# Optimization experiments

Hardware: AMD Instinct MI355X
Metric: run time of the kernel (lower is better)

The kernel has to match this reference:

```python
import jax, jax.numpy as jnp
import numpy as np

B, T, E, H, QKV = 4, 2048, 1024, 16, 64
D = E // H  # head_dim = 64


def setup_inputs() -> dict:
    key = jax.random.key(0)
    k1, k2, k3, k4 = jax.random.split(key, 4)
    scale = 1.0 / np.sqrt(D)
    x = jax.random.normal(k1, (B, T, E), dtype=jnp.float32)
    W_q = jax.random.normal(k2, (QKV, D), dtype=jnp.float32) * scale
    W_k = jax.random.normal(k3, (QKV, D), dtype=jnp.float32) * scale
    W_v = jax.random.normal(k4, (QKV, D), dtype=jnp.float32) * scale
    return {"x": x, "W_q": W_q, "W_k": W_k, "W_v": W_v}


def reference(x, W_q, W_k, W_v):
    Bx, Tx, Ex = x.shape
    d = Ex // H
    # [B,T,E] -> [B,H,T,D]  (same as torch view + permute(0,2,1,3))
    xh = x.reshape(Bx, Tx, H, d).transpose(0, 2, 1, 3)
    # Shared per-head projections: Linear(d -> qkv_dim), weight stored [out,in]
    Q = jnp.einsum("bhtd,qd->bhtq", xh, W_q)
    K = jnp.einsum("bhtd,qd->bhtq", xh, W_k)
    V = jnp.einsum("bhtd,qd->bhtq", xh, W_v)
    # NOTE: original scales by head_dim**0.5, not qkv_dim**0.5
    scores = jnp.einsum("bhtq,bhsq->bhts", Q, K) / jnp.asarray(d, x.dtype) ** 0.5
    attn = jax.nn.softmax(scores, axis=-1)
    out = jnp.einsum("bhts,bhsq->bhtq", attn, V) + V  # attention + V residual
    # per-head concat on last dim == head-major merge: [B,H,T,Q] -> [B,T,H*Q]
    return out.transpose(0, 2, 1, 3).reshape(Bx, Tx, H * W_q.shape[0])
```

## Files before the change

kernel.cpp:

```cpp
#include <hip/hip_runtime.h>

#define T_SEQ 2048
#define N_B   4
#define N_H   16
#define D_H   64
#define EMB   1024
#define CSC   0.18033688011f

typedef __attribute__((ext_vector_type(8))) short   vshort8;
typedef __attribute__((ext_vector_type(4))) float   vfloat4;
typedef __attribute__((ext_vector_type(16))) float  vfloat16;

__device__ __forceinline__ ushort f2bf(float f) {
  union { float f; unsigned u; } v; v.f = f;
  unsigned u = v.u;
  return (ushort)((u + 0x7fffu + ((u >> 16) & 1u)) >> 16);
}
__device__ __forceinline__ unsigned pk2bf(float a, float b) {
  return (unsigned)f2bf(a) | ((unsigned)f2bf(b) << 16);
}
__device__ __forceinline__ float bf2f(ushort b) {
  union { unsigned u; float f; } v; v.u = ((unsigned)b) << 16;
  return v.f;
}
__device__ __forceinline__ float fexp2(float x) {
#if __has_builtin(__builtin_amdgcn_exp2f)
  return __builtin_amdgcn_exp2f(x);
#else
  return exp2f(x);
#endif
}
__device__ __forceinline__ unsigned permhi(float hi, float lo) {
  union { float f; unsigned u; } a, b; a.f = hi; b.f = lo;
#if __has_builtin(__builtin_amdgcn_perm)
  return __builtin_amdgcn_perm(a.u, b.u, 0x07060302u);
#else
  return (a.u & 0xFFFF0000u) | (b.u >> 16);
#endif
}
__device__ __forceinline__ void plswap(unsigned &a, unsigned &b) {
  asm("v_permlane32_swap_b32 %0, %1" : "+v"(a), "+v"(b));
}
__device__ __forceinline__ vshort8 cvt8(const float* p) {
  float4 w0 = *(const float4*)(p);
  float4 w1 = *(const float4*)(p + 4);
  vshort8 t;
  t[0] = (short)f2bf(w0.x); t[1] = (short)f2bf(w0.y);
  t[2] = (short)f2bf(w0.z); t[3] = (short)f2bf(w0.w);
  t[4] = (short)f2bf(w1.x); t[5] = (short)f2bf(w1.y);
  t[6] = (short)f2bf(w1.z); t[7] = (short)f2bf(w1.w);
  return t;
}
__device__ __forceinline__ void gload_lds16(const uint4* gp, uint4* lp) {
  __builtin_amdgcn_global_load_lds(
      (const __attribute__((address_space(1))) void*)gp,
      (__attribute__((address_space(3))) void*)lp, 16, 0, 0);
}


__global__ void wconv(const float* __restrict__ Wq, const float* __restrict__ Wk,
                      const float* __restrict__ Wv, ushort* __restrict__ Wb) {
  const int lane = threadIdx.x & 63;
  const int l15  = lane & 15;
  const int quad = lane >> 4;
  const float* Ws[3] = {Wq, Wk, Wv};
#pragma unroll
  for (int m = 0; m < 3; ++m)
#pragma unroll
    for (int kc = 0; kc < 2; ++kc)
#pragma unroll
      for (int nt = 0; nt < 4; ++nt) {
        vshort8 t = cvt8(Ws[m] + (nt * 16 + l15) * D_H + kc * 32 + quad * 8);
        *(vshort8*)(&Wb[(((m * 2 + kc) * 4 + nt) * 64 + lane) * 8]) = t;
      }
}

__global__ __launch_bounds__(256, 4) void proj_qkv(
    const float* __restrict__ x, const ushort* __restrict__ Wb,
    uint2* __restrict__ Qb, uint2* __restrict__ Kb, uint2* __restrict__ Vb) {
  const int wid  = threadIdx.x >> 6;
  const int lane = threadIdx.x & 63;
  const int l15  = lane & 15;
  const int q    = lane >> 4;
  const int gw    = blockIdx.x * 4 + wid;
  const int strip = gw >> 4;
  const int hd    = gw & 15;
  const int r0    = strip * 16;
  const int b     = r0 >> 11;
  const int bh    = b * N_H + hd;
  const int ts    = (r0 & (T_SEQ - 1)) >> 4;

  vshort8 afr[2];
  {
    const float* xp = x + (size_t)(r0 + l15) * EMB + hd * D_H + q * 8;
    afr[0] = cvt8(xp);
    afr[1] = cvt8(xp + 32);
  }

  uint2* Bs[3] = {Qb, Kb, Vb};
#pragma unroll
  for (int m = 0; m < 3; ++m) {
    vshort8 wf[2][4];
#pragma unroll
    for (int kc = 0; kc < 2; ++kc)
#pragma unroll
      for (int nt = 0; nt < 4; ++nt)
        wf[kc][nt] = *(const vshort8*)(&Wb[(((m * 2 + kc) * 4 + nt) * 64 + lane) * 8]);
    vfloat4 acc[4];
#pragma unroll
    for (int nt = 0; nt < 4; ++nt) acc[nt] = (vfloat4){0.f, 0.f, 0.f, 0.f};
#pragma unroll
    for (int kc = 0; kc < 2; ++kc)
#pragma unroll
      for (int nt = 0; nt < 4; ++nt)
        acc[nt] = (m < 2)
          ? __builtin_amdgcn_mfma_f32_16x16x32_bf16(wf[kc][nt], afr[kc], acc[nt], 0, 0, 0)
          : __builtin_amdgcn_mfma_f32_16x16x32_bf16(afr[kc], wf[kc][nt], acc[nt], 0, 0, 0);
    uint2* B = Bs[m];
#pragma unroll
    for (int nt = 0; nt < 4; ++nt) {
      vfloat4 a = acc[nt];
      if (m == 0) { a[0] *= CSC; a[1] *= CSC; a[2] *= CSC; a[3] *= CSC; }
      uint2 w;
      w.x = pk2bf(a[0], a[1]);
      w.y = pk2bf(a[2], a[3]);
      size_t idx;
      if (m < 2) {
        idx = ((size_t)(bh * 64 + (ts >> 1)) * 4 + nt) * 128
              + (l15 + 16 * (ts & 1)) * 4 + q;
      } else {
        idx = (((size_t)(bh * 32 + (ts >> 2)) * 4 + (ts & 3)) * 2 + (nt >> 1)) * 128
              + 64 * (nt & 1) + l15 * 4 + q;
      }
      B[idx] = w;
    }
  }
}

__global__ __launch_bounds__(256, 2) void attn_fused(
    const uint4* __restrict__ Qb, const uint4* __restrict__ Kb,
    const uint4* __restrict__ Vb, float* __restrict__ out) {
  const int tid  = threadIdx.x;
  const int wid  = tid >> 6;
  const int lane = tid & 63;
  const int l31  = lane & 31;
  const int h    = lane >> 5;

  const int blk  = blockIdx.x;
  const int work = (blk & 7) * 64 + (blk >> 3);
  const int bh   = work >> 3;
  const int tblk8 = work & 7;
  const int b = bh >> 4, hh = bh & 15;
  const int T64 = tblk8 * 4 + wid;

  const int lo = l31 * 2 + h;

  __shared__ uint4 sK[2][512];

  const uint4* gp = Kb + (size_t)bh * 16384 + wid * 128 + lo;
  uint4* ldsA = &sK[0][wid * 128];
  uint4* ldsB = &sK[1][wid * 128];

  gload_lds16(gp, ldsA);
  gload_lds16(gp + 64, ldsA + 64);
  gp += 512;

  vshort8 qf[2][4];
#pragma unroll
  for (int tb = 0; tb < 2; ++tb)
#pragma unroll
    for (int ds = 0; ds < 4; ++ds)
      qf[tb][ds] = *(const vshort8*)&Qb[((size_t)(bh * 64 + 2 * T64 + tb) * 4 + ds) * 64 + lo];

  vfloat16 oacc[2][2];
#pragma unroll
  for (int tb = 0; tb < 2; ++tb)
#pragma unroll
    for (int db = 0; db < 2; ++db)
#pragma unroll
      for (int i = 0; i < 16; ++i) oacc[tb][db][i] = 0.f;
  float lsum[2] = {0.f, 0.f};

  __syncthreads();

#pragma unroll 1
  for (int ss = 0; ss < 32; ++ss) {
    if (ss < 31) {
      uint4* ld = (ss & 1) ? ldsA : ldsB;
      gload_lds16(gp, ld);
      gload_lds16(gp + 64, ld + 64);
      gp += 512;
    }

    vshort8 vf[4][2];
#pragma unroll
    for (int st = 0; st < 4; ++st)
#pragma unroll
      for (int db = 0; db < 2; ++db)
        vf[st][db] = *(const vshort8*)&Vb[(((size_t)(bh * 32 + ss) * 4 + st) * 2 + db) * 64 + lo];

    const uint4* lb = sK[ss & 1];
    vshort8 kf[2][4];
#pragma unroll
    for (int sb = 0; sb < 2; ++sb)
#pragma unroll
      for (int ds = 0; ds < 4; ++ds)
        kf[sb][ds] = *(const vshort8*)&lb[(sb * 4 + ds) * 64 + lane];

#pragma unroll
    for (int tb = 0; tb < 2; ++tb) {
      vfloat16 sacc[2];
#pragma unroll
      for (int sb = 0; sb < 2; ++sb)
#pragma unroll
        for (int i = 0; i < 16; ++i) sacc[sb][i] = 0.f;
      __builtin_amdgcn_s_setprio(1);
#pragma unroll
      for (int sb = 0; sb < 2; ++sb)
#pragma unroll
        for (int ds = 0; ds < 4; ++ds)
          sacc[sb] = __builtin_amdgcn_mfma_f32_32x32x16_bf16(kf[sb][ds], qf[tb][ds], sacc[sb], 0, 0, 0);
      __builtin_amdgcn_s_setprio(0);

      float p[2][16];
      float s0 = 0.f, s1 = 0.f, s2 = 0.f, s3 = 0.f;
#pragma unroll
      for (int sb = 0; sb < 2; ++sb)
#pragma unroll
        for (int r = 0; r < 16; r += 4) {
          p[sb][r + 0] = fexp2(sacc[sb][r + 0]); s0 += p[sb][r + 0];
          p[sb][r + 1] = fexp2(sacc[sb][r + 1]); s1 += p[sb][r + 1];
          p[sb][r + 2] = fexp2(sacc[sb][r + 2]); s2 += p[sb][r + 2];
          p[sb][r + 3] = fexp2(sacc[sb][r + 3]); s3 += p[sb][r + 3];
        }
      lsum[tb] += (s0 + s1) + (s2 + s3);

#pragma unroll
      for (int sb = 0; sb < 2; ++sb)
#pragma unroll
        for (int g = 0; g < 2; ++g) {
          unsigned OL0 = permhi(p[sb][8 * g + 1], p[sb][8 * g + 0]);
          unsigned OL1 = permhi(p[sb][8 * g + 3], p[sb][8 * g + 2]);
          unsigned OH0 = permhi(p[sb][8 * g + 5], p[sb][8 * g + 4]);
          unsigned OH1 = permhi(p[sb][8 * g + 7], p[sb][8 * g + 6]);
          plswap(OL0, OH0);
          plswap(OL1, OH1);
          union { unsigned u[4]; vshort8 v; } pa;
          pa.u[0] = OL0; pa.u[1] = OL1; pa.u[2] = OH0; pa.u[3] = OH1;
          const int st = 2 * sb + g;
          __builtin_amdgcn_s_setprio(1);
#pragma unroll
          for (int db = 0; db < 2; ++db)
            oacc[tb][db] = __builtin_amdgcn_mfma_f32_32x32x16_bf16(pa.v, vf[st][db], oacc[tb][db], 0, 0, 0);
          __builtin_amdgcn_s_setprio(0);
        }
    }

    __syncthreads();
  }

  const uint2* Vb2 = (const uint2*)Vb;
#pragma unroll
  for (int tb = 0; tb < 2; ++tb) {
    const float l = lsum[tb] + __shfl_xor(lsum[tb], 32, 64);
    const float inv = 1.0f / l;
    const int T32 = 2 * T64 + tb;
#pragma unroll
    for (int db = 0; db < 2; ++db) {
#pragma unroll
      for (int rq = 0; rq < 4; ++rq) {
        const int sq = 8 * T32 + 2 * rq + h;
        uint2 vr = Vb2[(((size_t)(bh * 32 + (sq >> 4)) * 4 + ((sq >> 2) & 3)) * 2 + db) * 128
                       + l31 * 4 + ((sq >> 1) & 1) * 2 + (sq & 1)];
        float vres[4];
        vres[0] = bf2f((ushort)(vr.x & 0xFFFFu));
        vres[1] = bf2f((ushort)(vr.x >> 16));
        vres[2] = bf2f((ushort)(vr.y & 0xFFFFu));
        vres[3] = bf2f((ushort)(vr.y >> 16));
#pragma unroll
        for (int rr = 0; rr < 4; ++rr) {
          const int row = rr + 8 * rq + 4 * h;
          const float iT = __shfl(inv, row, 64);
          const int t = T32 * 32 + row;
          out[((size_t)(b * T_SEQ + t)) * EMB + hh * D_H + db * 32 + l31] =
              oacc[tb][db][rq * 4 + rr] * iT + vres[rr];
        }
      }
    }
  }
}

extern "C" void kernel_launch(void* const* d_in, const int* in_sizes, int n_in,
                              void* d_out, int out_size, void* d_ws, size_t ws_size,
                              hipStream_t stream) {
  const float* x  = (const float*)d_in[0];
  const float* Wq = (const float*)d_in[1];
  const float* Wk = (const float*)d_in[2];
  const float* Wv = (const float*)d_in[3];
  float* out = (float*)d_out;

  const size_t per4 = (size_t)64 * 64 * 4 * 64;
  uint4* Qb = (uint4*)d_ws;
  uint4* Kb = Qb + per4;
  uint4* Vb = Kb + per4;
  ushort* Wb = (ushort*)(Vb + per4);

  wconv<<<1, 64, 0, stream>>>(Wq, Wk, Wv, Wb);
  proj_qkv<<<2048, 256, 0, stream>>>(x, Wb, (uint2*)Qb, (uint2*)Kb, (uint2*)Vb);
  attn_fused<<<512, 256, 0, stream>>>(Qb, Kb, Vb, out);
}
```

Measured before the change: 181.9 us.

## Fold weight conversion into projection kernel and load K directly from global

```diff
diff --git a/kernel.cpp b/kernel.cpp
--- a/kernel.cpp
+++ b/kernel.cpp
@@ -51,32 +51,11 @@
   t[6] = (short)f2bf(w1.z); t[7] = (short)f2bf(w1.w);
   return t;
 }
-__device__ __forceinline__ void gload_lds16(const uint4* gp, uint4* lp) {
-  __builtin_amdgcn_global_load_lds(
-      (const __attribute__((address_space(1))) void*)gp,
-      (__attribute__((address_space(3))) void*)lp, 16, 0, 0);
-}
-
-
-__global__ void wconv(const float* __restrict__ Wq, const float* __restrict__ Wk,
-                      const float* __restrict__ Wv, ushort* __restrict__ Wb) {
-  const int lane = threadIdx.x & 63;
-  const int l15  = lane & 15;
-  const int quad = lane >> 4;
-  const float* Ws[3] = {Wq, Wk, Wv};
-#pragma unroll
-  for (int m = 0; m < 3; ++m)
-#pragma unroll
-    for (int kc = 0; kc < 2; ++kc)
-#pragma unroll
-      for (int nt = 0; nt < 4; ++nt) {
-        vshort8 t = cvt8(Ws[m] + (nt * 16 + l15) * D_H + kc * 32 + quad * 8);
-        *(vshort8*)(&Wb[(((m * 2 + kc) * 4 + nt) * 64 + lane) * 8]) = t;
-      }
-}
+
 
 __global__ __launch_bounds__(256, 4) void proj_qkv(
-    const float* __restrict__ x, const ushort* __restrict__ Wb,
+    const float* __restrict__ x, const float* __restrict__ Wq,
+    const float* __restrict__ Wk, const float* __restrict__ Wv,
     uint2* __restrict__ Qb, uint2* __restrict__ Kb, uint2* __restrict__ Vb) {
   const int wid  = threadIdx.x >> 6;
   const int lane = threadIdx.x & 63;
@@ -90,12 +69,23 @@
   const int bh    = b * N_H + hd;
   const int ts    = (r0 & (T_SEQ - 1)) >> 4;
 
+  __shared__ ushort Wl[24 * 64 * 8];
+#pragma unroll
+  for (int fi = 0; fi < 6; ++fi) {
+    const int f  = wid + fi * 4;
+    const int m  = f >> 3, kc = (f >> 2) & 1, nt = f & 3;
+    const float* wsrc = (m == 0) ? Wq : (m == 1) ? Wk : Wv;
+    vshort8 t = cvt8(wsrc + (nt * 16 + l15) * D_H + kc * 32 + q * 8);
+    *(vshort8*)(&Wl[(f * 64 + lane) * 8]) = t;
+  }
+
   vshort8 afr[2];
   {
     const float* xp = x + (size_t)(r0 + l15) * EMB + hd * D_H + q * 8;
     afr[0] = cvt8(xp);
     afr[1] = cvt8(xp + 32);
   }
+  __syncthreads();
 
   uint2* Bs[3] = {Qb, Kb, Vb};
 #pragma unroll
@@ -105,7 +95,7 @@
     for (int kc = 0; kc < 2; ++kc)
 #pragma unroll
       for (int nt = 0; nt < 4; ++nt)
-        wf[kc][nt] = *(const vshort8*)(&Wb[(((m * 2 + kc) * 4 + nt) * 64 + lane) * 8]);
+        wf[kc][nt] = *(const vshort8*)(&Wl[(((m * 2 + kc) * 4 + nt) * 64 + lane) * 8]);
     vfloat4 acc[4];
 #pragma unroll
     for (int nt = 0; nt < 4; ++nt) acc[nt] = (vfloat4){0.f, 0.f, 0.f, 0.f};
@@ -155,16 +145,6 @@
 
   const int lo = l31 * 2 + h;
 
-  __shared__ uint4 sK[2][512];
-
-  const uint4* gp = Kb + (size_t)bh * 16384 + wid * 128 + lo;
-  uint4* ldsA = &sK[0][wid * 128];
-  uint4* ldsB = &sK[1][wid * 128];
-
-  gload_lds16(gp, ldsA);
-  gload_lds16(gp + 64, ldsA + 64);
-  gp += 512;
-
   vshort8 qf[2][4];
 #pragma unroll
   for (int tb = 0; tb < 2; ++tb)
@@ -181,31 +161,20 @@
       for (int i = 0; i < 16; ++i) oacc[tb][db][i] = 0.f;
   float lsum[2] = {0.f, 0.f};
 
-  __syncthreads();
-
 #pragma unroll 1
   for (int ss = 0; ss < 32; ++ss) {
-    if (ss < 31) {
-      uint4* ld = (ss & 1) ? ldsA : ldsB;
-      gload_lds16(gp, ld);
-      gload_lds16(gp + 64, ld + 64);
-      gp += 512;
-    }
-
+    vshort8 kf[2][4];
+#pragma unroll
+    for (int sb = 0; sb < 2; ++sb)
+#pragma unroll
+      for (int ds = 0; ds < 4; ++ds)
+        kf[sb][ds] = *(const vshort8*)&Kb[((size_t)(bh * 64 + 2 * ss + sb) * 4 + ds) * 64 + lo];
     vshort8 vf[4][2];
 #pragma unroll
     for (int st = 0; st < 4; ++st)
 #pragma unroll
       for (int db = 0; db < 2; ++db)
         vf[st][db] = *(const vshort8*)&Vb[(((size_t)(bh * 32 + ss) * 4 + st) * 2 + db) * 64 + lo];
-
-    const uint4* lb = sK[ss & 1];
-    vshort8 kf[2][4];
-#pragma unroll
-    for (int sb = 0; sb < 2; ++sb)
-#pragma unroll
-      for (int ds = 0; ds < 4; ++ds)
-        kf[sb][ds] = *(const vshort8*)&lb[(sb * 4 + ds) * 64 + lane];
 
 #pragma unroll
     for (int tb = 0; tb < 2; ++tb) {
@@ -255,8 +224,6 @@
           __builtin_amdgcn_s_setprio(0);
         }
     }
-
-    __syncthreads();
   }
 
   const uint2* Vb2 = (const uint2*)Vb;
@@ -303,9 +270,8 @@
   uint4* Qb = (uint4*)d_ws;
   uint4* Kb = Qb + per4;
   uint4* Vb = Kb + per4;
-  ushort* Wb = (ushort*)(Vb + per4);
-
-  wconv<<<1, 64, 0, stream>>>(Wq, Wk, Wv, Wb);
-  proj_qkv<<<2048, 256, 0, stream>>>(x, Wb, (uint2*)Qb, (uint2*)Kb, (uint2*)Vb);
+
+  proj_qkv<<<2048, 256, 0, stream>>>(x, Wq, Wk, Wv,
+                                     (uint2*)Qb, (uint2*)Kb, (uint2*)Vb);
   attn_fused<<<512, 256, 0, stream>>>(Qb, Kb, Vb, out);
 }
```

Result: faster. 176.7 us (-2.9%).
